# Kernel optimization log

Hardware: AMD Instinct MI355X
Metric: run time of the kernel (lower is better)

Reference implementation:

```python
import jax, jax.numpy as jnp
import numpy as np

K = 5          # kernel_size per dim
B = 100        # batch size (hard-coded in source)
GRID = 28
NUM_FIRST_FC = 49  # adjs[2].size(0) = 7*7


def spline_conv(x, edge_index, pseudo, W, root, bias):
    """Degree-1 open B-spline graph conv (SplineGCN).
    x: [N, Cin]; edge_index: [2, E] (src, dst); pseudo: [E, 2] in [0,1];
    W: [K*K, Cin, Cout]; root: [Cin, Cout]; bias: [Cout].
    out_i = mean_{j->i} sum_taps b_tap(u_ij) * (x_j @ W[k_tap]) + x_i @ root + bias
    """
    N = x.shape[0]
    src, dst = edge_index[0], edge_index[1]
    pos = pseudo * (K - 1)                     # open spline: scale to [0, K-1]
    kf = jnp.floor(pos)
    frac = pos - kf                            # [E, 2]
    k0 = kf.astype(jnp.int32)
    k1 = jnp.minimum(k0 + 1, K - 1)
    # Precompute x @ W[k] for all 25 kernel indices: [N, K*K, Cout]
    y = jnp.einsum('ni,kio->nko', x, W)
    fx, fy = frac[:, 0], frac[:, 1]
    taps = [
        (k0[:, 0], k0[:, 1], (1 - fx) * (1 - fy)),
        (k0[:, 0], k1[:, 1], (1 - fx) * fy),
        (k1[:, 0], k0[:, 1], fx * (1 - fy)),
        (k1[:, 0], k1[:, 1], fx * fy),
    ]
    msg = jnp.zeros((src.shape[0], W.shape[2]), dtype=x.dtype)
    for ax, ay, w in taps:
        msg = msg + w[:, None] * y[src, ax * K + ay]   # gather [E, Cout]
    agg = jax.ops.segment_sum(msg, dst, num_segments=N)
    deg = jax.ops.segment_sum(jnp.ones_like(msg[:, 0]), dst, num_segments=N)
    return agg / jnp.maximum(deg, 1.0)[:, None] + x @ root + bias


def max_pool2(x):  # x: [b, H, W, C] -> [b, H/2, W/2, C] (same math as NCHW pool)
    b, h, w, c = x.shape
    return x.reshape(b, h // 2, 2, w // 2, 2, c).max(axis=(2, 4))


def setup_inputs() -> dict:
    key = jax.random.key(0)
    ks = jax.random.split(key, 16)
    N0, N1 = B * GRID * GRID, B * (GRID // 2) * (GRID // 2)
    E0, E1 = N0 * 8, N1 * 8
    s = 0.1
    return {
        'x': jax.random.normal(ks[0], (N0, 1), dtype=jnp.float32),
        'pseudo0': jax.random.uniform(ks[1], (E0, 2), dtype=jnp.float32),
        'pseudo1': jax.random.uniform(ks[2], (E1, 2), dtype=jnp.float32),
        'W1': jax.random.normal(ks[3], (K * K, 1, 32), dtype=jnp.float32) * s,
        'root1': jax.random.normal(ks[4], (1, 32), dtype=jnp.float32) * s,
        'b1': jnp.zeros((32,), dtype=jnp.float32),
        'W2': jax.random.normal(ks[5], (K * K, 32, 64), dtype=jnp.float32) * s,
        'root2': jax.random.normal(ks[6], (32, 64), dtype=jnp.float32) * s,
        'b2': jnp.zeros((64,), dtype=jnp.float32),
        'fc1_w': jax.random.normal(ks[7], (NUM_FIRST_FC * 64, 512), dtype=jnp.float32) * 0.02,
        'fc1_b': jnp.zeros((512,), dtype=jnp.float32),
        'fc2_w': jax.random.normal(ks[8], (512, 10), dtype=jnp.float32) * 0.02,
        'fc2_b': jnp.zeros((10,), dtype=jnp.float32),
        'edge_index0': jax.random.randint(ks[9], (2, E0), 0, N0, dtype=jnp.int32),
        'edge_index1': jax.random.randint(ks[10], (2, E1), 0, N1, dtype=jnp.int32),
    }


def reference(x, pseudo0, pseudo1, W1, root1, b1, W2, root2, b2,
              fc1_w, fc1_b, fc2_w, fc2_b, edge_index0, edge_index1):
    elu = jax.nn.elu
    # conv1 on 28x28 grid graph
    h = elu(spline_conv(x, edge_index0, pseudo0, W1, root1, b1))   # [B*784, 32]
    h = h.reshape(-1, GRID, GRID, 32)                              # [B, 28, 28, 32]
    h = max_pool2(h)                                               # [B, 14, 14, 32]
    h = h.reshape(-1, 32)                                          # [B*196, 32]
    # conv2 on 14x14 grid graph
    h = elu(spline_conv(h, edge_index1, pseudo1, W2, root2, b2))   # [B*196, 64]
    # faithful replication of the source's reshapes: (B*196) rows -> (B/4, 28, 28, 64)
    h = h.reshape(-1, GRID, GRID, 64)                              # [25, 28, 28, 64]
    h = max_pool2(h)                                               # [25, 14, 14, 64]
    h = h.reshape(-1, NUM_FIRST_FC * 64)                           # [100, 3136]
    h = elu(h @ fc1_w + fc1_b)
    # F.dropout with training=False (eval) is identity
    h = elu(h @ fc2_w + fc2_b)
    return jax.nn.log_softmax(h, axis=-1)
```

## Files before the change

### kernel.cpp

```cpp
#include <hip/hip_runtime.h>
#include <hip/hip_bf16.h>

#define KK 5
constexpr int N0 = 78400;
constexpr int E0 = 627200;
constexpr int N1 = 19600;
constexpr int E1 = 156800;
constexpr int C1 = 32, C2 = 64;
constexpr int BSZ = 100;
constexpr int FC1_IN = 3136, FC1_OUT = 512;
constexpr int NKEYS = 98000;
constexpr int NCOARSE = 383;
constexpr int CAPB = 2400;
constexpr int KEXT = 832;
constexpr int ULS = 836;
constexpr int UBS = 856;
constexpr int CH2 = 192;
constexpr int CH1 = 640;
constexpr int KZ = 7;

typedef __attribute__((ext_vector_type(8))) short bf16x8;
typedef __attribute__((ext_vector_type(4))) float f32x4;

__device__ __forceinline__ unsigned short f2bf(float f) {
    union { float f; unsigned u; } v; v.f = f;
    unsigned u = v.u;
    unsigned r = (u + 0x7FFF + ((u >> 16) & 1)) >> 16;
    return (unsigned short)r;
}

__device__ __forceinline__ void taps4(float px, float py,
                                      int& a00, int& a01, int& a10, int& a11,
                                      float& fx, float& fy) {
    float kfx = floorf(px), kfy = floorf(py);
    fx = px - kfx; fy = py - kfy;
    int k0x = min(max((int)kfx, 0), KK - 1);
    int k0y = min(max((int)kfy, 0), KK - 1);
    int k1x = min(k0x + 1, KK - 1), k1y = min(k0y + 1, KK - 1);
    a00 = k0x * KK + k0y; a01 = k0x * KK + k1y;
    a10 = k1x * KK + k0y; a11 = k1x * KK + k1y;
}

__global__ void coarse_bin(const int* __restrict__ ei0, const int* __restrict__ ei1,
                           const float* __restrict__ ps0, const float* __restrict__ ps1,
                           int* __restrict__ gcur, int2* __restrict__ pk2,
                           const float* __restrict__ fc1w, const float* __restrict__ W2,
                           const float* __restrict__ root2,
                           unsigned short* __restrict__ wt1,
                           unsigned short* __restrict__ w2t) {
    __shared__ int hist[NCOARSE];
    __shared__ int gbase[NCOARSE];
    __shared__ unsigned short tile[64 * 66];
    int t = threadIdx.x;
    if (blockIdx.x >= 192) {
        int pb = blockIdx.x - 192;
        if (pb >= 392) {
            int base = (pb - 392) * 6656;
            for (int i2 = t; i2 < 6656; i2 += 512) {
                int idx = base + i2;
                int o = idx / KEXT, k = idx - o * KEXT;
                float v = (k < 800) ? W2[k * 64 + o] : root2[(k - 800) * 64 + o];
                w2t[idx] = f2bf(v);
            }
            return;
        }
        int k0 = (pb >> 3) * 64, j0 = (pb & 7) * 64;
        int jj = t & 63, ks = t >> 6;
        for (int kk = ks; kk < 64; kk += 8)
            tile[kk * 66 + jj] = f2bf(fc1w[(k0 + kk) * FC1_OUT + j0 + jj]);
        __syncthreads();
        int kk2 = t & 63, js = t >> 6;
        for (int j2 = js; j2 < 64; j2 += 8)
            wt1[(j0 + j2) * FC1_IN + k0 + kk2] = tile[kk2 * 66 + j2];
        return;
    }
    for (int i = t; i < NCOARSE; i += 512) hist[i] = 0;
    __syncthreads();
    int e0b = blockIdx.x * 4096;
    int keys[8], rnk[8], pay0[8], pay1[8];
#pragma unroll
    for (int j = 0; j < 8; j++) {
        int e = e0b + t + j * 512;
        int gk = -1, p0 = 0, p1v = 0;
        if (e < E0) {
            gk = ei0[E0 + e];
            float px = ps0[2 * e] * 4.f, py = ps0[2 * e + 1] * 4.f;
            unsigned ux = min((unsigned)(px * 16384.f + 0.5f), 65535u);
            unsigned uy = min((unsigned)(py * 16384.f + 0.5f), 65535u);
            p0 = ei0[e]; p1v = (int)(ux | (uy << 16));
        } else if (e < E0 + E1) {
            int el = e - E0;
            gk = N0 + ei1[E1 + el];
            float px = ps1[2 * el] * 4.f, py = ps1[2 * el + 1] * 4.f;
            unsigned ux = min((unsigned)(px * 16384.f + 0.5f), 65535u);
            unsigned uy = min((unsigned)(py * 16384.f + 0.5f), 65535u);
            p0 = ei1[el]; p1v = (int)(ux | (uy << 16));
        }
        keys[j] = gk; pay0[j] = p0; pay1[j] = p1v;
    }
#pragma unroll
    for (int j = 0; j < 8; j++)
        if (keys[j] >= 0) rnk[j] = atomicAdd(&hist[keys[j] >> 8], 1);
    __syncthreads();
    for (int i = t; i < NCOARSE; i += 512)
        gbase[i] = hist[i] ? atomicAdd(&gcur[i], hist[i]) : 0;
    __syncthreads();
#pragma unroll
    for (int j = 0; j < 8; j++) {
        if (keys[j] >= 0) {
            int b = keys[j] >> 8;
            int p = gbase[b] + rnk[j];
            if (p < CAPB)
                pk2[b * CAPB + p] = make_int2(pay0[j] | ((keys[j] & 255) << 20), pay1[j]);
        }
    }
}

__global__ void fine_sort(const int2* __restrict__ pk2, const int* __restrict__ gcur,
                          int2* __restrict__ erec, int* __restrict__ off) {
    __shared__ int cl[NCOARSE];
    __shared__ int2 ent[CAPB];
    __shared__ int rnk[CAPB];
    __shared__ int h2[256];
    __shared__ int sc[256];
    __shared__ int redbuf[4];
    __shared__ int baseS;
    int b = blockIdx.x, t = threadIdx.x;
    for (int i2 = t; i2 < NCOARSE; i2 += 256) cl[i2] = min(gcur[i2], CAPB);
    __syncthreads();
    {
        int s = 0;
        if (t < b) s += cl[t];
        if (t + 256 < b) s += cl[t + 256];
#pragma unroll
        for (int o2 = 32; o2 > 0; o2 >>= 1) s += __shfl_down(s, o2);
        if ((t & 63) == 0) redbuf[t >> 6] = s;
        __syncthreads();
        if (t == 0) baseS = redbuf[0] + redbuf[1] + redbuf[2] + redbuf[3];
        __syncthreads();
    }
    int base = baseS;
    int cb = cl[b];
    h2[t] = 0;
    __syncthreads();
    for (int i = t; i < cb; i += 256) {
        int2 v = pk2[b * CAPB + i];
        ent[i] = v;
        rnk[i] = atomicAdd(&h2[(v.x >> 20) & 255], 1);
    }
    __syncthreads();
    int v0 = h2[t];
    sc[t] = v0;
    __syncthreads();
    for (int d = 1; d < 256; d <<= 1) {
        int add = (t >= d) ? sc[t - d] : 0;
        __syncthreads();
        sc[t] += add;
        __syncthreads();
    }
    int excl = sc[t] - v0;
    __syncthreads();
    sc[t] = excl;
    __syncthreads();
    int n = (b << 8) + t;
    if (n < NKEYS) off[n] = base + excl;
    if (b == 0 && t == 0) off[NKEYS] = E0 + E1;
    for (int i = t; i < cb; i += 256) {
        int2 v = ent[i];
        erec[base + sc[(v.x >> 20) & 255] + rnk[i]] = v;
    }
}

__global__ __launch_bounds__(256, 4)
void conv1_pool(const int2* __restrict__ erec, const int* __restrict__ off,
                const float* __restrict__ x,
                const float* __restrict__ W1,
                const float* __restrict__ root, const float* __restrict__ bias,
                float* __restrict__ p1) {
    __shared__ float S4[224 * 25];
    __shared__ float Sr[56 * 25];
    __shared__ float exv[CH1], efx[CH1], efy[CH1];
    __shared__ int   emt[CH1];
    float* h1t = S4;
    int t = threadIdx.x;
    int bb = blockIdx.x;
    int n0 = bb * 56;
    int q = t & 3, nl = t >> 2;
    bool actN = nl < 56;
    int n = n0 + (actN ? nl : 0);
    float* sp = S4 + (actN ? (nl * 4 + q) : 0) * 25;
    for (int i = t; i < 224 * 25; i += 256) S4[i] = 0.f;
    int e0 = off[n0], e1 = off[n0 + 56];
    int my0 = off[n], my1 = off[n + 1];
    for (int base = e0; base < e1; base += CH1) {
        int nE = min(e1 - base, CH1);
        __syncthreads();
        for (int j = t; j < nE; j += 256) {
            int2 r = erec[base + j];
            int src = r.x & 0xFFFFF;
            float px = (float)((unsigned)r.y & 0xFFFF) * (1.f / 16384.f);
            float py = (float)((unsigned)r.y >> 16) * (1.f / 16384.f);
            int a00, a01, a10, a11; float fx, fy;
            taps4(px, py, a00, a01, a10, a11, fx, fy);
            emt[j] = a00 | (a01 << 5) | (a10 << 10) | (a11 << 15);
            efx[j] = fx; efy[j] = fy;
            exv[j] = x[src];
        }
        __syncthreads();
        if (actN) {
            int r0 = max(my0 - base, 0), r1 = min(my1 - base, nE);
            for (int p = r0 + q; p < r1; p += 4) {
                float xv = exv[p]; int m = emt[p];
                float fx = efx[p], fy = efy[p];
                float gx = 1.f - fx, gy = 1.f - fy;
                sp[m & 31]         += gx * gy * xv;
                sp[(m >> 5) & 31]  += gx * fy * xv;
                sp[(m >> 10) & 31] += fx * gy * xv;
                sp[(m >> 15) & 31] += fx * fy * xv;
            }
        }
    }
    __syncthreads();
    for (int i2 = t; i2 < 56 * 25; i2 += 256) {
        int n2 = i2 / 25, a = i2 - n2 * 25;
        Sr[i2] = S4[(n2 * 4 + 0) * 25 + a] + S4[(n2 * 4 + 1) * 25 + a] +
                 S4[(n2 * 4 + 2) * 25 + a] + S4[(n2 * 4 + 3) * 25 + a];
    }
    __syncthreads();
    {
        int o = t & 31, ng = t >> 5;
        float w1c[25];
#pragma unroll
        for (int a = 0; a < 25; a++) w1c[a] = W1[a * C1 + o];
        float ro = root[o], bo = bias[o];
        for (int j2 = 0; j2 < 7; j2++) {
            int nl2 = ng * 7 + j2;
            int n2 = n0 + nl2;
            float acc = 0.f;
#pragma unroll
            for (int a = 0; a < 25; a++) acc += Sr[nl2 * 25 + a] * w1c[a];
            float invd = 1.f / fmaxf((float)(off[n2 + 1] - off[n2]), 1.f);
            float v = acc * invd + x[n2] * ro + bo;
            h1t[nl2 * 32 + o] = v > 0.f ? v : expm1f(v);
        }
    }
    __syncthreads();
    for (int i2 = t; i2 < 448; i2 += 256) {
        int o2 = i2 & 31, pc = i2 >> 5;
        float m0 = h1t[(2 * pc) * 32 + o2],      m1 = h1t[(2 * pc + 1) * 32 + o2];
        float m2 = h1t[(28 + 2 * pc) * 32 + o2], m3 = h1t[(28 + 2 * pc + 1) * 32 + o2];
        p1[(bb * 14 + pc) * C1 + o2] = fmaxf(fmaxf(m0, m1), fmaxf(m2, m3));
    }
}

__global__ __launch_bounds__(512, 4)
void conv2_fused(const float* __restrict__ p1, const int2* __restrict__ erec,
                 const int* __restrict__ off,
                 const unsigned short* __restrict__ w2t,
                 const float* __restrict__ b2, float* __restrict__ h2) {
    __shared__ float Ul[16 * ULS];
    __shared__ int   es[CH2];
    __shared__ int   et[CH2];
    __shared__ float efx[CH2], efy[CH2];
    unsigned short* Ub = (unsigned short*)Ul;
    int t = threadIdx.x;
    int nb = blockIdx.x * 16;
    int i = t & 31;
    int g = t >> 5;
    float* up = Ul + g * ULS;
#pragma unroll
    for (int a = 0; a < 25; a++) up[a * 32 + i] = 0.f;
    up[800 + i] = p1[(nb + g) * C1 + i];
    int e0 = off[N0 + nb], e1 = off[N0 + nb + 16];
    int my0 = off[N0 + nb + g], my1 = off[N0 + nb + g + 1];
    for (int base = e0; base < e1; base += CH2) {
        int nE = min(e1 - base, CH2);
        __syncthreads();
        for (int j = t; j < nE; j += 512) {
            int2 r = erec[base + j];
            es[j] = r.x & 0xFFFFF;
            float px = (float)((unsigned)r.y & 0xFFFF) * (1.f / 16384.f);
            float py = (float)((unsigned)r.y >> 16) * (1.f / 16384.f);
            int a00, a01, a10, a11; float fx, fy;
            taps4(px, py, a00, a01, a10, a11, fx, fy);
            et[j] = a00 | (a01 << 5) | (a10 << 10) | (a11 << 15);
            efx[j] = fx; efy[j] = fy;
        }
        __syncthreads();
        int r0 = max(my0 - base, 0);
        int r1 = min(my1 - base, nE);
        int cnt = max(r1 - r0, 0);
        int m4 = max(cnt, __shfl_xor(cnt, 32));
        for (int jj = 0; jj < m4; jj += 4) {
            bool a0 = jj < cnt, a1 = jj + 1 < cnt, a2 = jj + 2 < cnt, a3 = jj + 3 < cnt;
            int j0 = a0 ? r0 + jj     : 0;
            int j1 = a1 ? r0 + jj + 1 : 0;
            int j2 = a2 ? r0 + jj + 2 : 0;
            int j3 = a3 ? r0 + jj + 3 : 0;
            int s0 = es[j0], s1 = es[j1], s2 = es[j2], s3 = es[j3];
            int mm0 = et[j0], mm1 = et[j1], mm2 = et[j2], mm3 = et[j3];
            float fx0 = efx[j0], fy0 = efy[j0];
            float fx1 = efx[j1], fy1 = efy[j1];
            float fx2 = efx[j2], fy2 = efy[j2];
            float fx3 = efx[j3], fy3 = efy[j3];
            float x0 = p1[s0 * C1 + i];
            float x1 = p1[s1 * C1 + i];
            float x2 = p1[s2 * C1 + i];
            float x3 = p1[s3 * C1 + i];
            if (a0) {
                float gx = 1.f - fx0, gy = 1.f - fy0;
                up[(mm0 & 31) * 32 + i]         += gx * gy * x0;
                up[((mm0 >> 5) & 31) * 32 + i]  += gx * fy0 * x0;
                up[((mm0 >> 10) & 31) * 32 + i] += fx0 * gy * x0;
                up[((mm0 >> 15) & 31) * 32 + i] += fx0 * fy0 * x0;
            }
            if (a1) {
                float gx = 1.f - fx1, gy = 1.f - fy1;
                up[(mm1 & 31) * 32 + i]         += gx * gy * x1;
                up[((mm1 >> 5) & 31) * 32 + i]  += gx * fy1 * x1;
                up[((mm1 >> 10) & 31) * 32 + i] += fx1 * gy * x1;
                up[((mm1 >> 15) & 31) * 32 + i] += fx1 * fy1 * x1;
            }
            if (a2) {
                float gx = 1.f - fx2, gy = 1.f - fy2;
                up[(mm2 & 31) * 32 + i]         += gx * gy * x2;
                up[((mm2 >> 5) & 31) * 32 + i]  += gx * fy2 * x2;
                up[((mm2 >> 10) & 31) * 32 + i] += fx2 * gy * x2;
                up[((mm2 >> 15) & 31) * 32 + i] += fx2 * fy2 * x2;
            }
            if (a3) {
                float gx = 1.f - fx3, gy = 1.f - fy3;
                up[(mm3 & 31) * 32 + i]         += gx * gy * x3;
                up[((mm3 >> 5) & 31) * 32 + i]  += gx * fy3 * x3;
                up[((mm3 >> 10) & 31) * 32 + i] += fx3 * gy * x3;
                up[((mm3 >> 15) & 31) * 32 + i] += fx3 * fy3 * x3;
            }
        }
    }
    __syncthreads();
    {
        int g2 = t >> 5, i2c = t & 31;
        int dgc = off[N0 + nb + g2 + 1] - off[N0 + nb + g2];
        float invd = 1.f / fmaxf((float)dgc, 1.f);
        const float* srcp = Ul + g2 * ULS + i2c * 26;
        float rv[26];
#pragma unroll
        for (int j = 0; j < 26; j++) {
            float v = srcp[j];
            rv[j] = (i2c * 26 + j < 800) ? v * invd : v;
        }
        __syncthreads();
        unsigned* dstp = (unsigned*)(Ub + g2 * UBS + i2c * 26);
#pragma unroll
        for (int j = 0; j < 13; j++) {
            unsigned lo = f2bf(rv[2 * j]), hi = f2bf(rv[2 * j + 1]);
            dstp[j] = lo | (hi << 16);
        }
    }
    __syncthreads();
    int wv = t >> 6, lane = t & 63, quad = lane >> 4, lrow = lane & 15;
    if (wv < 4) {
        f32x4 acc = {0.f, 0.f, 0.f, 0.f};
        const unsigned short* bbase = w2t + (wv * 16 + lrow) * KEXT;
        const unsigned short* abase = Ub + lrow * UBS;
#pragma unroll
        for (int kc = 0; kc < 26; kc++) {
            bf16x8 a = *(const bf16x8*)(abase + kc * 32 + quad * 8);
            bf16x8 b = *(const bf16x8*)(bbase + kc * 32 + quad * 8);
            acc = __builtin_amdgcn_mfma_f32_16x16x32_bf16(a, b, acc, 0, 0, 0);
        }
        int o = wv * 16 + lrow;
        float bo = b2[o];
#pragma unroll
        for (int r = 0; r < 4; r++) {
            int node = quad * 4 + r;
            float v = acc[r] + bo;
            v = v > 0.f ? v : expm1f(v);
            h2[(nb + node) * C2 + o] = v;
        }
    }
}

__global__ void pool2b(const float* __restrict__ h2, unsigned short* __restrict__ p2b) {
    int idx = blockIdx.x * blockDim.x + threadIdx.x;
    if (idx >= 112 * FC1_IN) return;
    if (idx >= 100 * FC1_IN) { p2b[idx] = 0; return; }
    int o = idx & 63; int t2 = idx >> 6;
    int c = t2 % 14; int r = (t2 / 14) % 14; int b = t2 / 196;
    const float* base = h2 + (((b * 28 + 2 * r) * 28 + 2 * c) * C2 + o);
    float m = fmaxf(fmaxf(base[0], base[C2]),
                    fmaxf(base[28 * C2], base[28 * C2 + C2]));
    p2b[idx] = f2bf(m);
}

__global__ void gemm_fc1(const unsigned short* __restrict__ p2b,
                         const unsigned short* __restrict__ wt1,
                         float* __restrict__ z1p) {
    constexpr int AS = 232;
    __shared__ unsigned short as_[16 * AS];
    int t = threadIdx.x;
    int jt = blockIdx.x, mt = blockIdx.y, kz = blockIdx.z;
    int wv = t >> 6, lane = t & 63, quad = lane >> 4, lrow = lane & 15;
    int m0 = mt * 16;
    int kbase = kz * 448;
    const unsigned short* bbase = wt1 + (jt * 64 + wv * 16 + lrow) * FC1_IN + kbase;
    f32x4 acc = {0.f, 0.f, 0.f, 0.f};
    for (int ch = 0; ch < 2; ch++) {
        __syncthreads();
        for (int slot = t; slot < 448; slot += 256) {
            int r = slot / 28, c = slot - (slot / 28) * 28;
            *(uint4*)(as_ + r * AS + c * 8) =
                *(const uint4*)(p2b + (m0 + r) * FC1_IN + kbase + ch * 224 + c * 8);
        }
        __syncthreads();
        const unsigned short* ab = as_ + lrow * AS;
        const unsigned short* bb = bbase + ch * 224;
#pragma unroll
        for (int kk = 0; kk < 7; kk++) {
            bf16x8 a = *(const bf16x8*)(ab + kk * 32 + quad * 8);
            bf16x8 b = *(const bf16x8*)(bb + kk * 32 + quad * 8);
            acc = __builtin_amdgcn_mfma_f32_16x16x32_bf16(a, b, acc, 0, 0, 0);
        }
    }
    int n = jt * 64 + wv * 16 + lrow;
#pragma unroll
    for (int r = 0; r < 4; r++) {
        int m = m0 + quad * 4 + r;
        z1p[kz * (112 * FC1_OUT) + m * FC1_OUT + n] = acc[r];
    }
}

__global__ void fc2_lsm(const float* __restrict__ z1p, const float* __restrict__ fc1b,
                        const float* __restrict__ w, const float* __restrict__ fc2b,
                        float* __restrict__ out) {
    int b = blockIdx.x;
    int t = threadIdx.x;
    int wv = t >> 6;
    int lane = t & 63;
    float acc = 0.f;
#pragma unroll
    for (int m = 0; m < 8; m++) {
        int k = lane * 8 + m;
        float xv = fc1b[k];
#pragma unroll
        for (int p = 0; p < KZ; p++)
            xv += z1p[p * (112 * FC1_OUT) + b * FC1_OUT + k];
        xv = xv > 0.f ? xv : expm1f(xv);
        acc += xv * w[k * 10 + wv];
    }
#pragma unroll
    for (int off = 32; off > 0; off >>= 1) acc += __shfl_down(acc, off);
    __shared__ float zs[10];
    if (lane == 0) {
        float z = acc + fc2b[wv];
        zs[wv] = z > 0.f ? z : expm1f(z);
    }
    __syncthreads();
    if (t < 10) {
        float m = -1e30f;
        for (int jj = 0; jj < 10; jj++) m = fmaxf(m, zs[jj]);
        float s = 0.f;
        for (int jj = 0; jj < 10; jj++) s += expf(zs[jj] - m);
        out[b * 10 + t] = zs[t] - m - logf(s);
    }
}

extern "C" void kernel_launch(void* const* d_in, const int* in_sizes, int n_in,
                              void* d_out, int out_size, void* d_ws, size_t ws_size,
                              hipStream_t stream) {
    const float* x     = (const float*)d_in[0];
    const float* ps0   = (const float*)d_in[1];
    const float* ps1   = (const float*)d_in[2];
    const float* W1    = (const float*)d_in[3];
    const float* root1 = (const float*)d_in[4];
    const float* b1    = (const float*)d_in[5];
    const float* W2    = (const float*)d_in[6];
    const float* root2 = (const float*)d_in[7];
    const float* b2v   = (const float*)d_in[8];
    const float* fc1w  = (const float*)d_in[9];
    const float* fc1b  = (const float*)d_in[10];
    const float* fc2w  = (const float*)d_in[11];
    const float* fc2b  = (const float*)d_in[12];
    const int*   ei0   = (const int*)d_in[13];
    const int*   ei1   = (const int*)d_in[14];

    float* ws = (float*)d_ws;
    int*  gcur = (int*)ws;
    int*  off  = (int*)(ws + 384);
    int2* pk2  = (int2*)(ws + 98388);
    int2* erec = (int2*)(ws + 1936788);
    float* p1  = ws + 3504788;
    float* h2  = ws + 4131988;
    unsigned short* p2b = (unsigned short*)(ws + 5386388);
    float* z1p = ws + 5474196;
    unsigned short* w2t = (unsigned short*)(ws + 5875604);
    unsigned short* wt1 = (unsigned short*)(ws + 5888916);

    hipMemsetAsync(gcur, 0, (size_t)NCOARSE * sizeof(int), stream);

    coarse_bin<<<592, 512, 0, stream>>>(ei0, ei1, ps0, ps1, gcur, pk2,
                                        fc1w, W2, root2, wt1, w2t);
    fine_sort<<<NCOARSE, 256, 0, stream>>>(pk2, gcur, erec, off);
    conv1_pool<<<1400, 256, 0, stream>>>(erec, off, x, W1, root1, b1, p1);
    conv2_fused<<<N1 / 16, 512, 0, stream>>>(p1, erec, off, w2t, b2v, h2);
    pool2b<<<(112 * FC1_IN + 255) / 256, 256, 0, stream>>>(h2, p2b);
    gemm_fc1<<<dim3(8, 7, KZ), 256, 0, stream>>>(p2b, wt1, z1p);
    fc2_lsm<<<BSZ, 640, 0, stream>>>(z1p, fc1b, fc2w, fc2b, (float*)d_out);
}
```

Measured before the change: 201.2 us.

## Replace conv1 edge sort with fixed-point atomic scatter, split-bf16 fc1 GEMM

Conv1 edges are no longer sorted. Each edge scatters its four spline-weighted x contributions and a degree count into a per-node 26-slot integer accumulator with fixed-point atomics, and a dense conv1 kernel then reads those rows. Only conv2 edges go through the bin/fine-sort pipeline, which now stores full-float pseudo coordinates and the edge id. Fine_sort gains a serial per-node rank pass to make the edge order deterministic. The fc1 GEMM switches to hi/lo bf16 splits with three MFMAs per step for near-fp32 accuracy, which adds extra memory traffic and compute, and the memset grows to about 8 MB.

```diff
diff --git a/kernel.cpp b/kernel.cpp
--- a/kernel.cpp
+++ b/kernel.cpp
@@ -9,15 +9,21 @@
 constexpr int C1 = 32, C2 = 64;
 constexpr int BSZ = 100;
 constexpr int FC1_IN = 3136, FC1_OUT = 512;
-constexpr int NKEYS = 98000;
-constexpr int NCOARSE = 383;
+constexpr int NC1 = 77;
 constexpr int CAPB = 2400;
 constexpr int KEXT = 832;
 constexpr int ULS = 836;
 constexpr int UBS = 856;
 constexpr int CH2 = 192;
-constexpr int CH1 = 640;
 constexpr int KZ = 7;
+
+constexpr float SC22  = 4194304.f;
+constexpr float ISC22 = 1.f / 4194304.f;
+
+constexpr int BIN_BLKS  = 39;
+constexpr int WT1_BLKS  = 392;
+constexpr int W2T_BLKS  = 8;
+constexpr int SCAT_BLKS = 613;
 
 typedef __attribute__((ext_vector_type(8))) short bf16x8;
 typedef __attribute__((ext_vector_type(4))) float f32x4;
@@ -27,6 +33,9 @@
     unsigned u = v.u;
     unsigned r = (u + 0x7FFF + ((u >> 16) & 1)) >> 16;
     return (unsigned short)r;
+}
+__device__ __forceinline__ float bf2f(unsigned short h) {
+    return __uint_as_float(((unsigned)h) << 16);
 }
 
 __device__ __forceinline__ void taps4(float px, float py,
@@ -43,19 +52,46 @@
 
 __global__ void coarse_bin(const int* __restrict__ ei0, const int* __restrict__ ei1,
                            const float* __restrict__ ps0, const float* __restrict__ ps1,
-                           int* __restrict__ gcur, int2* __restrict__ pk2,
+                           const float* __restrict__ x,
+                           int* __restrict__ U0i,
+                           int* __restrict__ gcur, int4* __restrict__ pk4,
                            const float* __restrict__ fc1w, const float* __restrict__ W2,
                            const float* __restrict__ root2,
-                           unsigned short* __restrict__ wt1,
+                           unsigned short* __restrict__ wt1h,
+                           unsigned short* __restrict__ wt1l,
                            unsigned short* __restrict__ w2t) {
-    __shared__ int hist[NCOARSE];
-    __shared__ int gbase[NCOARSE];
-    __shared__ unsigned short tile[64 * 66];
+    __shared__ int hist[NC1];
+    __shared__ int gbase[NC1];
+    __shared__ float tilef[64 * 66];
     int t = threadIdx.x;
-    if (blockIdx.x >= 192) {
-        int pb = blockIdx.x - 192;
-        if (pb >= 392) {
-            int base = (pb - 392) * 6656;
+    int bx = blockIdx.x;
+    if (bx >= 439) {
+        int pb = bx - 439;
+        const float2* ps0v = (const float2*)ps0;
+#pragma unroll
+        for (int half = 0; half < 2; half++) {
+            int e = pb * 1024 + t + half * 512;
+            if (e < E0) {
+                int src = ei0[e], dst = ei0[E0 + e];
+                float2 pv = ps0v[e];
+                float xv = x[src];
+                int a00, a01, a10, a11; float fx, fy;
+                taps4(pv.x * 4.f, pv.y * 4.f, a00, a01, a10, a11, fx, fy);
+                float gx = 1.f - fx, gy = 1.f - fy;
+                int* row = U0i + dst * 26;
+                atomicAdd(row + a00, __float2int_rn(gx * gy * xv * SC22));
+                atomicAdd(row + a01, __float2int_rn(gx * fy * xv * SC22));
+                atomicAdd(row + a10, __float2int_rn(fx * gy * xv * SC22));
+                atomicAdd(row + a11, __float2int_rn(fx * fy * xv * SC22));
+                atomicAdd(row + 25, 1);
+            }
+        }
+        return;
+    }
+    if (bx >= 39) {
+        int pb = bx - 39;
+        if (pb >= WT1_BLKS) {
+            int base = (pb - WT1_BLKS) * 6656;
             for (int i2 = t; i2 < 6656; i2 += 512) {
                 int idx = base + i2;
                 int o = idx / KEXT, k = idx - o * KEXT;
@@ -67,42 +103,40 @@
         int k0 = (pb >> 3) * 64, j0 = (pb & 7) * 64;
         int jj = t & 63, ks = t >> 6;
         for (int kk = ks; kk < 64; kk += 8)
-            tile[kk * 66 + jj] = f2bf(fc1w[(k0 + kk) * FC1_OUT + j0 + jj]);
+            tilef[kk * 66 + jj] = fc1w[(k0 + kk) * FC1_OUT + j0 + jj];
         __syncthreads();
         int kk2 = t & 63, js = t >> 6;
-        for (int j2 = js; j2 < 64; j2 += 8)
-            wt1[(j0 + j2) * FC1_IN + k0 + kk2] = tile[kk2 * 66 + j2];
+        for (int j2 = js; j2 < 64; j2 += 8) {
+            float v = tilef[kk2 * 66 + j2];
+            unsigned short h = f2bf(v);
+            int idx = (j0 + j2) * FC1_IN + k0 + kk2;
+            wt1h[idx] = h;
+            wt1l[idx] = f2bf(v - bf2f(h));
+        }
         return;
     }
-    for (int i = t; i < NCOARSE; i += 512) hist[i] = 0;
-    __syncthreads();
-    int e0b = blockIdx.x * 4096;
-    int keys[8], rnk[8], pay0[8], pay1[8];
+    for (int i = t; i < NC1; i += 512) hist[i] = 0;
+    __syncthreads();
+    int e0b = bx * 4096;
+    const float2* ps1v = (const float2*)ps1;
+    int keys[8], rnk[8], psrc[8], peid[8]; float ppx[8], ppy[8];
 #pragma unroll
     for (int j = 0; j < 8; j++) {
         int e = e0b + t + j * 512;
-        int gk = -1, p0 = 0, p1v = 0;
-        if (e < E0) {
-            gk = ei0[E0 + e];
-            float px = ps0[2 * e] * 4.f, py = ps0[2 * e + 1] * 4.f;
-            unsigned ux = min((unsigned)(px * 16384.f + 0.5f), 65535u);
-            unsigned uy = min((unsigned)(py * 16384.f + 0.5f), 65535u);
-            p0 = ei0[e]; p1v = (int)(ux | (uy << 16));
-        } else if (e < E0 + E1) {
-            int el = e - E0;
-            gk = N0 + ei1[E1 + el];
-            float px = ps1[2 * el] * 4.f, py = ps1[2 * el + 1] * 4.f;
-            unsigned ux = min((unsigned)(px * 16384.f + 0.5f), 65535u);
-            unsigned uy = min((unsigned)(py * 16384.f + 0.5f), 65535u);
-            p0 = ei1[el]; p1v = (int)(ux | (uy << 16));
-        }
-        keys[j] = gk; pay0[j] = p0; pay1[j] = p1v;
+        int gk = -1, p0 = 0; float px = 0.f, py = 0.f;
+        if (e < E1) {
+            gk = ei1[E1 + e];
+            float2 pv = ps1v[e];
+            px = pv.x * 4.f; py = pv.y * 4.f;
+            p0 = ei1[e];
+        }
+        keys[j] = gk; psrc[j] = p0; peid[j] = e; ppx[j] = px; ppy[j] = py;
     }
 #pragma unroll
     for (int j = 0; j < 8; j++)
         if (keys[j] >= 0) rnk[j] = atomicAdd(&hist[keys[j] >> 8], 1);
     __syncthreads();
-    for (int i = t; i < NCOARSE; i += 512)
+    for (int i = t; i < NC1; i += 512)
         gbase[i] = hist[i] ? atomicAdd(&gcur[i], hist[i]) : 0;
     __syncthreads();
 #pragma unroll
@@ -111,27 +145,29 @@
             int b = keys[j] >> 8;
             int p = gbase[b] + rnk[j];
             if (p < CAPB)
-                pk2[b * CAPB + p] = make_int2(pay0[j] | ((keys[j] & 255) << 20), pay1[j]);
-        }
-    }
-}
-
-__global__ void fine_sort(const int2* __restrict__ pk2, const int* __restrict__ gcur,
-                          int2* __restrict__ erec, int* __restrict__ off) {
-    __shared__ int cl[NCOARSE];
-    __shared__ int2 ent[CAPB];
+                pk4[b * CAPB + p] = make_int4(psrc[j] | ((keys[j] & 255) << 20),
+                                              __float_as_int(ppx[j]),
+                                              __float_as_int(ppy[j]), peid[j]);
+        }
+    }
+}
+
+__global__ void fine_sort(const int4* __restrict__ pk4, const int* __restrict__ gcur,
+                          int4* __restrict__ erec, int* __restrict__ off) {
+    __shared__ int cl[NC1];
+    __shared__ int4 ent[CAPB];
+    __shared__ int4 ent2[CAPB];
     __shared__ int rnk[CAPB];
     __shared__ int h2[256];
     __shared__ int sc[256];
     __shared__ int redbuf[4];
     __shared__ int baseS;
     int b = blockIdx.x, t = threadIdx.x;
-    for (int i2 = t; i2 < NCOARSE; i2 += 256) cl[i2] = min(gcur[i2], CAPB);
+    for (int i2 = t; i2 < NC1; i2 += 256) cl[i2] = min(gcur[i2], CAPB);
     __syncthreads();
     {
         int s = 0;
         if (t < b) s += cl[t];
-        if (t + 256 < b) s += cl[t + 256];
 #pragma unroll
         for (int o2 = 32; o2 > 0; o2 >>= 1) s += __shfl_down(s, o2);
         if ((t & 63) == 0) redbuf[t >> 6] = s;
@@ -144,7 +180,7 @@
     h2[t] = 0;
     __syncthreads();
     for (int i = t; i < cb; i += 256) {
-        int2 v = pk2[b * CAPB + i];
+        int4 v = pk4[b * CAPB + i];
         ent[i] = v;
         rnk[i] = atomicAdd(&h2[(v.x >> 20) & 255], 1);
     }
@@ -163,69 +199,33 @@
     sc[t] = excl;
     __syncthreads();
     int n = (b << 8) + t;
-    if (n < NKEYS) off[n] = base + excl;
-    if (b == 0 && t == 0) off[NKEYS] = E0 + E1;
-    for (int i = t; i < cb; i += 256) {
-        int2 v = ent[i];
-        erec[base + sc[(v.x >> 20) & 255] + rnk[i]] = v;
-    }
-}
-
-__global__ __launch_bounds__(256, 4)
-void conv1_pool(const int2* __restrict__ erec, const int* __restrict__ off,
-                const float* __restrict__ x,
-                const float* __restrict__ W1,
-                const float* __restrict__ root, const float* __restrict__ bias,
-                float* __restrict__ p1) {
-    __shared__ float S4[224 * 25];
-    __shared__ float Sr[56 * 25];
-    __shared__ float exv[CH1], efx[CH1], efy[CH1];
-    __shared__ int   emt[CH1];
-    float* h1t = S4;
+    if (n < N1) off[n] = base + excl;
+    if (b == 0 && t == 0) off[N1] = E1;
+    for (int i = t; i < cb; i += 256)
+        ent2[sc[(ent[i].x >> 20) & 255] + rnk[i]] = ent[i];
+    __syncthreads();
+    {
+        int s = sc[t];
+        for (int i = 0; i < v0; i++) {
+            int4 a = ent2[s + i];
+            int rank = 0;
+            for (int j = 0; j < v0; j++) rank += (ent2[s + j].w < a.w) ? 1 : 0;
+            erec[base + s + rank] = a;
+        }
+    }
+}
+
+__global__ __launch_bounds__(256, 8)
+void conv1_dense(const int* __restrict__ U0i, const float* __restrict__ x,
+                 const float* __restrict__ W1, const float* __restrict__ root,
+                 const float* __restrict__ bias, float* __restrict__ p1) {
+    __shared__ int   Sri[56 * 26];
+    __shared__ float h1t[56 * 32];
     int t = threadIdx.x;
     int bb = blockIdx.x;
     int n0 = bb * 56;
-    int q = t & 3, nl = t >> 2;
-    bool actN = nl < 56;
-    int n = n0 + (actN ? nl : 0);
-    float* sp = S4 + (actN ? (nl * 4 + q) : 0) * 25;
-    for (int i = t; i < 224 * 25; i += 256) S4[i] = 0.f;
-    int e0 = off[n0], e1 = off[n0 + 56];
-    int my0 = off[n], my1 = off[n + 1];
-    for (int base = e0; base < e1; base += CH1) {
-        int nE = min(e1 - base, CH1);
-        __syncthreads();
-        for (int j = t; j < nE; j += 256) {
-            int2 r = erec[base + j];
-            int src = r.x & 0xFFFFF;
-            float px = (float)((unsigned)r.y & 0xFFFF) * (1.f / 16384.f);
-            float py = (float)((unsigned)r.y >> 16) * (1.f / 16384.f);
-            int a00, a01, a10, a11; float fx, fy;
-            taps4(px, py, a00, a01, a10, a11, fx, fy);
-            emt[j] = a00 | (a01 << 5) | (a10 << 10) | (a11 << 15);
-            efx[j] = fx; efy[j] = fy;
-            exv[j] = x[src];
-        }
-        __syncthreads();
-        if (actN) {
-            int r0 = max(my0 - base, 0), r1 = min(my1 - base, nE);
-            for (int p = r0 + q; p < r1; p += 4) {
-                float xv = exv[p]; int m = emt[p];
-                float fx = efx[p], fy = efy[p];
-                float gx = 1.f - fx, gy = 1.f - fy;
-                sp[m & 31]         += gx * gy * xv;
-                sp[(m >> 5) & 31]  += gx * fy * xv;
-                sp[(m >> 10) & 31] += fx * gy * xv;
-                sp[(m >> 15) & 31] += fx * fy * xv;
-            }
-        }
-    }
-    __syncthreads();
-    for (int i2 = t; i2 < 56 * 25; i2 += 256) {
-        int n2 = i2 / 25, a = i2 - n2 * 25;
-        Sr[i2] = S4[(n2 * 4 + 0) * 25 + a] + S4[(n2 * 4 + 1) * 25 + a] +
-                 S4[(n2 * 4 + 2) * 25 + a] + S4[(n2 * 4 + 3) * 25 + a];
-    }
+    for (int i2 = t; i2 < 56 * 26; i2 += 256)
+        Sri[i2] = U0i[n0 * 26 + i2];
     __syncthreads();
     {
         int o = t & 31, ng = t >> 5;
@@ -234,14 +234,15 @@
         for (int a = 0; a < 25; a++) w1c[a] = W1[a * C1 + o];
         float ro = root[o], bo = bias[o];
         for (int j2 = 0; j2 < 7; j2++) {
-            int nl2 = ng * 7 + j2;
-            int n2 = n0 + nl2;
+            int nl = ng * 7 + j2;
+            int n = n0 + nl;
             float acc = 0.f;
 #pragma unroll
-            for (int a = 0; a < 25; a++) acc += Sr[nl2 * 25 + a] * w1c[a];
-            float invd = 1.f / fmaxf((float)(off[n2 + 1] - off[n2]), 1.f);
-            float v = acc * invd + x[n2] * ro + bo;
-            h1t[nl2 * 32 + o] = v > 0.f ? v : expm1f(v);
+            for (int a = 0; a < 25; a++) acc += (float)Sri[nl * 26 + a] * w1c[a];
+            float dg = (float)Sri[nl * 26 + 25];
+            float invd = ISC22 / fmaxf(dg, 1.f);
+            float v = acc * invd + x[n] * ro + bo;
+            h1t[nl * 32 + o] = v > 0.f ? v : expm1f(v);
         }
     }
     __syncthreads();
@@ -254,7 +255,7 @@
 }
 
 __global__ __launch_bounds__(512, 4)
-void conv2_fused(const float* __restrict__ p1, const int2* __restrict__ erec,
+void conv2_fused(const float* __restrict__ p1, const int4* __restrict__ erec,
                  const int* __restrict__ off,
                  const unsigned short* __restrict__ w2t,
                  const float* __restrict__ b2, float* __restrict__ h2) {
@@ -271,16 +272,16 @@
 #pragma unroll
     for (int a = 0; a < 25; a++) up[a * 32 + i] = 0.f;
     up[800 + i] = p1[(nb + g) * C1 + i];
-    int e0 = off[N0 + nb], e1 = off[N0 + nb + 16];
-    int my0 = off[N0 + nb + g], my1 = off[N0 + nb + g + 1];
+    int e0 = off[nb], e1 = off[nb + 16];
+    int my0 = off[nb + g], my1 = off[nb + g + 1];
     for (int base = e0; base < e1; base += CH2) {
         int nE = min(e1 - base, CH2);
         __syncthreads();
         for (int j = t; j < nE; j += 512) {
-            int2 r = erec[base + j];
+            int4 r = erec[base + j];
             es[j] = r.x & 0xFFFFF;
-            float px = (float)((unsigned)r.y & 0xFFFF) * (1.f / 16384.f);
-            float py = (float)((unsigned)r.y >> 16) * (1.f / 16384.f);
+            float px = __int_as_float(r.y);
+            float py = __int_as_float(r.z);
             int a00, a01, a10, a11; float fx, fy;
             taps4(px, py, a00, a01, a10, a11, fx, fy);
             et[j] = a00 | (a01 << 5) | (a10 << 10) | (a11 << 15);
@@ -340,7 +341,7 @@
     __syncthreads();
     {
         int g2 = t >> 5, i2c = t & 31;
-        int dgc = off[N0 + nb + g2 + 1] - off[N0 + nb + g2];
+        int dgc = off[nb + g2 + 1] - off[nb + g2];
         float invd = 1.f / fmaxf((float)dgc, 1.f);
         const float* srcp = Ul + g2 * ULS + i2c * 26;
         float rv[26];
@@ -381,45 +382,61 @@
     }
 }
 
-__global__ void pool2b(const float* __restrict__ h2, unsigned short* __restrict__ p2b) {
+__global__ void pool2b(const float* __restrict__ h2,
+                       unsigned short* __restrict__ p2bh,
+                       unsigned short* __restrict__ p2bl) {
     int idx = blockIdx.x * blockDim.x + threadIdx.x;
     if (idx >= 112 * FC1_IN) return;
-    if (idx >= 100 * FC1_IN) { p2b[idx] = 0; return; }
+    if (idx >= 100 * FC1_IN) { p2bh[idx] = 0; p2bl[idx] = 0; return; }
     int o = idx & 63; int t2 = idx >> 6;
     int c = t2 % 14; int r = (t2 / 14) % 14; int b = t2 / 196;
     const float* base = h2 + (((b * 28 + 2 * r) * 28 + 2 * c) * C2 + o);
     float m = fmaxf(fmaxf(base[0], base[C2]),
                     fmaxf(base[28 * C2], base[28 * C2 + C2]));
-    p2b[idx] = f2bf(m);
-}
-
-__global__ void gemm_fc1(const unsigned short* __restrict__ p2b,
-                         const unsigned short* __restrict__ wt1,
+    unsigned short h = f2bf(m);
+    p2bh[idx] = h;
+    p2bl[idx] = f2bf(m - bf2f(h));
+}
+
+__global__ void gemm_fc1(const unsigned short* __restrict__ p2bh,
+                         const unsigned short* __restrict__ p2bl,
+                         const unsigned short* __restrict__ wt1h,
+                         const unsigned short* __restrict__ wt1l,
                          float* __restrict__ z1p) {
     constexpr int AS = 232;
-    __shared__ unsigned short as_[16 * AS];
+    __shared__ unsigned short ash[16 * AS];
+    __shared__ unsigned short asl[16 * AS];
     int t = threadIdx.x;
     int jt = blockIdx.x, mt = blockIdx.y, kz = blockIdx.z;
     int wv = t >> 6, lane = t & 63, quad = lane >> 4, lrow = lane & 15;
     int m0 = mt * 16;
     int kbase = kz * 448;
-    const unsigned short* bbase = wt1 + (jt * 64 + wv * 16 + lrow) * FC1_IN + kbase;
+    int brow = (jt * 64 + wv * 16 + lrow) * FC1_IN + kbase;
+    const unsigned short* bh0 = wt1h + brow;
+    const unsigned short* bl0 = wt1l + brow;
     f32x4 acc = {0.f, 0.f, 0.f, 0.f};
     for (int ch = 0; ch < 2; ch++) {
         __syncthreads();
         for (int slot = t; slot < 448; slot += 256) {
             int r = slot / 28, c = slot - (slot / 28) * 28;
-            *(uint4*)(as_ + r * AS + c * 8) =
-                *(const uint4*)(p2b + (m0 + r) * FC1_IN + kbase + ch * 224 + c * 8);
-        }
-        __syncthreads();
-        const unsigned short* ab = as_ + lrow * AS;
-        const unsigned short* bb = bbase + ch * 224;
+            int gsrc = (m0 + r) * FC1_IN + kbase + ch * 224 + c * 8;
+            *(uint4*)(ash + r * AS + c * 8) = *(const uint4*)(p2bh + gsrc);
+            *(uint4*)(asl + r * AS + c * 8) = *(const uint4*)(p2bl + gsrc);
+        }
+        __syncthreads();
+        const unsigned short* abh = ash + lrow * AS;
+        const unsigned short* abl = asl + lrow * AS;
+        const unsigned short* bbh = bh0 + ch * 224;
+        const unsigned short* bbl = bl0 + ch * 224;
 #pragma unroll
         for (int kk = 0; kk < 7; kk++) {
-            bf16x8 a = *(const bf16x8*)(ab + kk * 32 + quad * 8);
-            bf16x8 b = *(const bf16x8*)(bb + kk * 32 + quad * 8);
-            acc = __builtin_amdgcn_mfma_f32_16x16x32_bf16(a, b, acc, 0, 0, 0);
+            bf16x8 ah = *(const bf16x8*)(abh + kk * 32 + quad * 8);
+            bf16x8 al = *(const bf16x8*)(abl + kk * 32 + quad * 8);
+            bf16x8 bh = *(const bf16x8*)(bbh + kk * 32 + quad * 8);
+            bf16x8 bl = *(const bf16x8*)(bbl + kk * 32 + quad * 8);
+            acc = __builtin_amdgcn_mfma_f32_16x16x32_bf16(ah, bh, acc, 0, 0, 0);
+            acc = __builtin_amdgcn_mfma_f32_16x16x32_bf16(ah, bl, acc, 0, 0, 0);
+            acc = __builtin_amdgcn_mfma_f32_16x16x32_bf16(al, bh, acc, 0, 0, 0);
         }
     }
     int n = jt * 64 + wv * 16 + lrow;
@@ -485,25 +502,28 @@
     const int*   ei1   = (const int*)d_in[14];
 
     float* ws = (float*)d_ws;
-    int*  gcur = (int*)ws;
-    int*  off  = (int*)(ws + 384);
-    int2* pk2  = (int2*)(ws + 98388);
-    int2* erec = (int2*)(ws + 1936788);
-    float* p1  = ws + 3504788;
-    float* h2  = ws + 4131988;
-    unsigned short* p2b = (unsigned short*)(ws + 5386388);
-    float* z1p = ws + 5474196;
-    unsigned short* w2t = (unsigned short*)(ws + 5875604);
-    unsigned short* wt1 = (unsigned short*)(ws + 5888916);
-
-    hipMemsetAsync(gcur, 0, (size_t)NCOARSE * sizeof(int), stream);
-
-    coarse_bin<<<592, 512, 0, stream>>>(ei0, ei1, ps0, ps1, gcur, pk2,
-                                        fc1w, W2, root2, wt1, w2t);
-    fine_sort<<<NCOARSE, 256, 0, stream>>>(pk2, gcur, erec, off);
-    conv1_pool<<<1400, 256, 0, stream>>>(erec, off, x, W1, root1, b1, p1);
+    int*   gcur = (int*)ws;
+    int*   U0i  = (int*)(ws + 384);
+    int*   off  = (int*)(ws + 2038784);
+    int4*  pk4  = (int4*)(ws + 2058400);
+    int4*  erec = (int4*)(ws + 2797600);
+    float* p1   = ws + 3424800;
+    float* h2   = ws + 4052000;
+    unsigned short* p2bh = (unsigned short*)(ws + 5306400);
+    unsigned short* p2bl = (unsigned short*)(ws + 5482016);
+    float* z1p  = ws + 5657632;
+    unsigned short* w2t  = (unsigned short*)(ws + 6059040);
+    unsigned short* wt1h = (unsigned short*)(ws + 6085664);
+    unsigned short* wt1l = (unsigned short*)(ws + 6888480);
+
+    hipMemsetAsync(gcur, 0, (size_t)(384 + 2038400) * sizeof(int), stream);
+
+    coarse_bin<<<BIN_BLKS + WT1_BLKS + W2T_BLKS + SCAT_BLKS, 512, 0, stream>>>(
+        ei0, ei1, ps0, ps1, x, U0i, gcur, pk4, fc1w, W2, root2, wt1h, wt1l, w2t);
+    fine_sort<<<NC1, 256, 0, stream>>>(pk4, gcur, erec, off);
+    conv1_dense<<<1400, 256, 0, stream>>>(U0i, x, W1, root1, b1, p1);
     conv2_fused<<<N1 / 16, 512, 0, stream>>>(p1, erec, off, w2t, b2v, h2);
-    pool2b<<<(112 * FC1_IN + 255) / 256, 256, 0, stream>>>(h2, p2b);
-    gemm_fc1<<<dim3(8, 7, KZ), 256, 0, stream>>>(p2b, wt1, z1p);
+    pool2b<<<(112 * FC1_IN + 255) / 256, 256, 0, stream>>>(h2, p2bh, p2bl);
+    gemm_fc1<<<dim3(8, 7, KZ), 256, 0, stream>>>(p2bh, p2bl, wt1h, wt1l, z1p);
     fc2_lsm<<<BSZ, 640, 0, stream>>>(z1p, fc1b, fc2w, fc2b, (float*)d_out);
 }
```

Result: slower. 324.0 us (+61.0%).
